# Performance work log

Measured on AMD Instinct MI355X. Metric: run time of the kernel, lower is better.

Reference implementation:

```python
import jax, jax.numpy as jnp
import numpy as np

D_MODEL = 1024
D_FFN = 4096
NUM_EXPERTS = 8
TOP_K = 2
EPS = 1e-7


def setup_inputs() -> dict:
    key = jax.random.key(0)
    ks = jax.random.split(key, 10)
    B, T = 2, 2048
    s = 0.02
    return {
        "x": jax.random.normal(ks[0], (B, T, D_MODEL), dtype=jnp.float32),
        "padding_mask": jnp.ones((B, T), dtype=bool),
        "rms_w": jnp.ones((D_MODEL,), dtype=jnp.float32),
        "router_w": jax.random.normal(ks[1], (NUM_EXPERTS, D_MODEL), dtype=jnp.float32) * s,
        "router_b": jnp.zeros((NUM_EXPERTS,), dtype=jnp.float32),
        "W1": jax.random.normal(ks[2], (NUM_EXPERTS, D_MODEL, D_FFN), dtype=jnp.float32) * s,
        "b1": jnp.zeros((NUM_EXPERTS, D_FFN), dtype=jnp.float32),
        "W2": jax.random.normal(ks[3], (NUM_EXPERTS, D_FFN, D_MODEL), dtype=jnp.float32) * s,
        "b2": jnp.zeros((NUM_EXPERTS, D_MODEL), dtype=jnp.float32),
        "W3": jax.random.normal(ks[4], (NUM_EXPERTS, D_MODEL, D_FFN), dtype=jnp.float32) * s,
        "b3": jnp.zeros((NUM_EXPERTS, D_FFN), dtype=jnp.float32),
    }


def reference(x, padding_mask, rms_w, router_w, router_b, W1, b1, W2, b2, W3, b3):
    B, T, d = x.shape
    # RMSNorm
    rms = jnp.sqrt(jnp.mean(x * x, axis=-1, keepdims=True) + EPS)
    xn = rms_w * (x / rms)
    xf = xn.reshape(-1, d)  # [N, d]

    # Router: softmax -> top-k -> renormalize
    logits = xf @ router_w.T + router_b            # [N, E]
    probs = jax.nn.softmax(logits, axis=-1)
    topv, topi = jax.lax.top_k(probs, TOP_K)       # [N, K]
    w = topv / jnp.sum(topv, axis=-1, keepdims=True)
    # Dense combine weights per (token, expert): sum of top-k weights routed to e
    combine = jnp.sum(jax.nn.one_hot(topi, NUM_EXPERTS, dtype=xf.dtype) * w[..., None], axis=1)  # [N, E]

    # Loop over experts via scan (one full-token SwiGLU FFN per expert, masked combine)
    def step(acc, params):
        W1e, b1e, W2e, b2e, W3e, b3e, ce = params
        h = jax.nn.silu(xf @ W1e + b1e) * (xf @ W3e + b3e)  # [N, d_ffn]
        y = h @ W2e + b2e                                    # [N, d]
        return acc + ce[:, None] * y, None

    out, _ = jax.lax.scan(step, jnp.zeros_like(xf), (W1, b1, W2, b2, W3, b3, combine.T))
    aux_loss = jnp.asarray(0.0, dtype=x.dtype)  # use_aux_loss only active in training mode
    return out.reshape(B, T, d), aux_loss
```

## Files before the change

kernel.cpp:

```cpp
#include <hip/hip_runtime.h>
#include <stdint.h>


#define NTOK 4096
#define DM   1024
#define DF   4096
#define NE   8
#define BM   128
#define MAX_RB 72
#define SLOT_CAP (MAX_RB * BM)

typedef _Float16 f16;
typedef __attribute__((ext_vector_type(8))) _Float16 f16x8;
typedef __attribute__((ext_vector_type(4))) _Float16 f16x4;
typedef __attribute__((ext_vector_type(4))) float    f32x4;
typedef __attribute__((ext_vector_type(2))) float    f32x2;

__device__ __forceinline__ void gl2lds16(const void* g, void* l) {
  __builtin_amdgcn_global_load_lds(
      (const __attribute__((address_space(1))) unsigned int*)g,
      (__attribute__((address_space(3))) unsigned int*)l, 16, 0, 0);
}

__global__ __launch_bounds__(256) void k_rms_router(
    const float* __restrict__ x, const float* __restrict__ rms_w,
    const float* __restrict__ rw, const float* __restrict__ rbias,
    f16* __restrict__ xn, int* __restrict__ topi, float* __restrict__ topw,
    int* __restrict__ counts)
{
  int t = blockIdx.x;
  int tid = threadIdx.x;
  const float* xr = x + (size_t)t * DM;
  f32x4 xv = *(const f32x4*)(xr + tid * 4);
  f32x4 gw = *(const f32x4*)(rms_w + tid * 4);
  f32x4 gv = xv * gw;

  float v[9];
  v[8] = xv[0]*xv[0] + xv[1]*xv[1] + xv[2]*xv[2] + xv[3]*xv[3];
#pragma unroll
  for (int e = 0; e < NE; ++e) {
    f32x4 wv = *(const f32x4*)(rw + e * DM + tid * 4);
    v[e] = gv[0]*wv[0] + gv[1]*wv[1] + gv[2]*wv[2] + gv[3]*wv[3];
  }
#pragma unroll
  for (int off = 32; off; off >>= 1) {
#pragma unroll
    for (int j = 0; j < 9; ++j) v[j] += __shfl_xor(v[j], off);
  }
  __shared__ float red[4][9];
  int wave = tid >> 6, lane = tid & 63;
  if (lane == 0) {
#pragma unroll
    for (int j = 0; j < 9; ++j) red[wave][j] = v[j];
  }
  __syncthreads();
  float tot[9];
#pragma unroll
  for (int j = 0; j < 9; ++j)
    tot[j] = red[0][j] + red[1][j] + red[2][j] + red[3][j];

  float rinv = 1.0f / sqrtf(tot[8] * (1.0f / DM) + 1e-7f);
  float lg[NE];
#pragma unroll
  for (int e = 0; e < NE; ++e) lg[e] = tot[e] * rinv + rbias[e];

  int e1 = 0; float b1v = lg[0];
#pragma unroll
  for (int e = 1; e < NE; ++e) if (lg[e] > b1v) { b1v = lg[e]; e1 = e; }
  int e2 = -1; float b2v = -1e30f;
#pragma unroll
  for (int e = 0; e < NE; ++e) if (e != e1 && lg[e] > b2v) { b2v = lg[e]; e2 = e; }

  float r2 = expf(b2v - b1v);
  float w1 = 1.0f / (1.0f + r2);
  float w2 = r2 * w1;

  if (tid == 0) {
    topi[t * 2 + 0] = e1; topi[t * 2 + 1] = e2;
    topw[t * 2 + 0] = w1; topw[t * 2 + 1] = w2;
    atomicAdd(&counts[e1], 1);
    atomicAdd(&counts[e2], 1);
  }
  f16x4 o;
#pragma unroll
  for (int i = 0; i < 4; ++i) o[i] = (f16)(gv[i] * rinv);
  *(f16x4*)(xn + (size_t)t * DM + tid * 4) = o;
}

__global__ void k_build(const int* __restrict__ counts, int* __restrict__ po,
                        int2* __restrict__ rbtable, int* __restrict__ total_rb)
{
  if (threadIdx.x != 0 || blockIdx.x != 0) return;
  int off = 0, idx = 0;
  for (int e = 0; e < NE; ++e) {
    int c = counts[e];
    po[e] = off;
    int nrb = (c + BM - 1) / BM;
    for (int r = 0; r < nrb; ++r) { rbtable[idx] = make_int2(e, off + r * BM); ++idx; }
    off += nrb * BM;
  }
  *total_rb = idx;
}

__global__ __launch_bounds__(256) void k_assign(
    const int* __restrict__ topi, const float* __restrict__ topw,
    const int* __restrict__ po, int* __restrict__ cursors,
    int* __restrict__ slot_token, float* __restrict__ slot_w,
    int* __restrict__ tok2slot)
{
  int t = blockIdx.x * 256 + threadIdx.x;
  if (t >= NTOK) return;
#pragma unroll
  for (int k = 0; k < 2; ++k) {
    int e = topi[t * 2 + k];
    int pos = atomicAdd(&cursors[e], 1);
    int slot = po[e] + pos;
    slot_token[slot] = t;
    slot_w[slot] = topw[t * 2 + k];
    tok2slot[t * 2 + k] = slot;
  }
}

__global__ __launch_bounds__(256) void k_convw(
    const float* __restrict__ W1, const float* __restrict__ W3,
    const float* __restrict__ W2, f16* __restrict__ w16)
{
  __shared__ f16 T[64][132];
  int g = blockIdx.x;
  int tensor = g >> 12;
  int rem = g & 4095;
  int e = rem >> 9;
  int t = rem & 511;
  const float* W; int nstride, np, kt;
  if (tensor == 2) { W = W2; nstride = DM; np = t >> 6; kt = t & 63; }
  else { W = (tensor == 0) ? W1 : W3; nstride = DF; np = t >> 4; kt = t & 15; }
  const float* src = W + (size_t)e * DM * DF + (size_t)(kt * 64) * nstride + np * 128;

  int tid = threadIdx.x;
  int q = tid & 31, kb = tid >> 5;
#pragma unroll
  for (int i = 0; i < 8; ++i) {
    int k = kb + 8 * i;
    f32x4 v = *(const f32x4*)(src + (size_t)k * nstride + q * 4);
    f16x4 h4 = { (f16)v[0], (f16)v[1], (f16)v[2], (f16)v[3] };
    *(f16x4*)(&T[k][q * 4]) = h4;
  }
  __syncthreads();
  int n = tid >> 1;
  f16* dst = w16 + ((size_t)(tensor * NE + e) * 512 + t) * 8192 + n * 64 + (tid & 1) * 32;
#pragma unroll
  for (int qq = 0; qq < 4; ++qq) {
    int cs = (tid & 1) * 4 + qq;
    int cl = cs ^ (n & 7);
    f16x8 o;
#pragma unroll
    for (int j = 0; j < 8; ++j) o[j] = T[cl * 8 + j][n];
    *(f16x8*)(dst + qq * 8) = o;
  }
}

__global__ __launch_bounds__(256, 3) void k_ffn13(
    const f16* __restrict__ xn, const int* __restrict__ slot_token,
    const int2* __restrict__ rbtable, const int* __restrict__ total_rb,
    const f16* __restrict__ w16,
    const float* __restrict__ b1, const float* __restrict__ b3,
    f16* __restrict__ h)
{
  int bid = blockIdx.x;
  int wl = (bid & 7) * 288 + (bid >> 3);
  int rbi = wl % 72;
  int np  = wl / 72;
  if (rbi >= *total_rb) return;
  int2 ent = rbtable[rbi];
  int e = ent.x, row0 = ent.y;
  int n0 = np * 128;

  __shared__ __align__(16) f16 As[128 * 64];
  __shared__ __align__(16) f16 Bs[2][128 * 64];

  int tid = threadIdx.x, lane = tid & 63, wave = tid >> 6;
  int wm = wave >> 1, wn = wave & 1;

  const f16* wb1 = w16 + ((size_t)(0 * NE + e) * 512 + np * 16) * 8192;
  const f16* wb3 = w16 + ((size_t)(1 * NE + e) * 512 + np * 16) * 8192;

  int tok[4];
#pragma unroll
  for (int q = 0; q < 4; ++q) {
    int m = q * 32 + wave * 8 + (lane >> 3);
    int tkn = slot_token[row0 + m];
    tok[q] = (tkn < 0) ? 0 : tkn;
  }
  int csx = (((lane & 7) ^ (lane >> 3)) << 3);
  int lin = wave * 512 + lane * 8;

  f32x4 acc1[4][4], acc3[4][4];
  f32x4 z = {0.f, 0.f, 0.f, 0.f};
#pragma unroll
  for (int i = 0; i < 4; ++i)
#pragma unroll
    for (int j = 0; j < 4; ++j) { acc1[i][j] = z; acc3[i][j] = z; }

  for (int kt = 0; kt < DM / 64; ++kt) {
    int k0 = kt * 64;
    const f16* s1 = wb1 + (size_t)kt * 8192;
    const f16* s3 = wb3 + (size_t)kt * 8192;
#pragma unroll
    for (int q = 0; q < 4; ++q) {
      gl2lds16(xn + (size_t)tok[q] * DM + k0 + csx,
               (char*)As + q * 4096 + wave * 1024);
      gl2lds16(s1 + q * 2048 + lin, (char*)Bs[0] + q * 4096 + wave * 1024);
      gl2lds16(s3 + q * 2048 + lin, (char*)Bs[1] + q * 4096 + wave * 1024);
    }
    __syncthreads();
#pragma unroll
    for (int kh = 0; kh < 2; ++kh) {
      int kk = kh * 32 + (lane >> 4) * 8;
      f16x8 a[4];
#pragma unroll
      for (int fm = 0; fm < 4; ++fm) {
        int m = wm * 64 + fm * 16 + (lane & 15);
        a[fm] = *(const f16x8*)((char*)As + m * 128 + 2 * (kk ^ ((m & 7) << 3)));
      }
#pragma unroll
      for (int fn = 0; fn < 4; ++fn) {
        int n = wn * 64 + fn * 16 + (lane & 15);
        f16x8 bf1 = *(const f16x8*)((char*)Bs[0] + n * 128 + 2 * (kk ^ ((n & 7) << 3)));
        f16x8 bf3 = *(const f16x8*)((char*)Bs[1] + n * 128 + 2 * (kk ^ ((n & 7) << 3)));
#pragma unroll
        for (int fm = 0; fm < 4; ++fm) {
          acc1[fm][fn] = __builtin_amdgcn_mfma_f32_16x16x32_f16(a[fm], bf1, acc1[fm][fn], 0, 0, 0);
          acc3[fm][fn] = __builtin_amdgcn_mfma_f32_16x16x32_f16(a[fm], bf3, acc3[fm][fn], 0, 0, 0);
        }
      }
    }
    __syncthreads();
  }
#pragma unroll
  for (int fn = 0; fn < 4; ++fn) {
    int nc = n0 + wn * 64 + fn * 16 + (lane & 15);
    float bb1 = b1[e * DF + nc], bb3 = b3[e * DF + nc];
#pragma unroll
    for (int fm = 0; fm < 4; ++fm) {
      int mbase = wm * 64 + fm * 16 + (lane >> 4) * 4;
#pragma unroll
      for (int r = 0; r < 4; ++r) {
        int sl = mbase + r;
        float u1 = acc1[fm][fn][r] + bb1;
        float u3 = acc3[fm][fn][r] + bb3;
        float hv = (u1 / (1.0f + __expf(-u1))) * u3;
        size_t off = (size_t)(row0 + sl) * DF + (nc & ~63)
                   + ((((nc >> 3) & 7) ^ (sl & 7)) << 3) + (nc & 7);
        h[off] = (f16)hv;
      }
    }
  }
}

__global__ __launch_bounds__(256, 4) void k_ffn2(
    const f16* __restrict__ h,
    const int2* __restrict__ rbtable, const int* __restrict__ total_rb,
    const f16* __restrict__ w16, f16* __restrict__ partial)
{
  int bid = blockIdx.x;
  int wl = (bid & 7) * 288 + (bid >> 3);
  int rbi = wl % 72;
  int rest = wl / 72;
  int kc = rest & 3;
  int np = rest >> 2;
  if (rbi >= *total_rb) return;
  int2 ent = rbtable[rbi];
  int e = ent.x, row0 = ent.y;
  int n0 = np * 128;

  __shared__ __align__(16) f16 As[128 * 64];
  __shared__ __align__(16) f16 Bsh[128 * 64];

  int tid = threadIdx.x, lane = tid & 63, wave = tid >> 6;
  int wm = wave >> 1, wn = wave & 1;
  const f16* wb = w16 + ((size_t)(2 * NE + e) * 512 + np * 64 + kc * 16) * 8192;
  int lin = wave * 512 + lane * 8;

  f32x4 acc[4][4];
  f32x4 z = {0.f, 0.f, 0.f, 0.f};
#pragma unroll
  for (int i = 0; i < 4; ++i)
#pragma unroll
    for (int j = 0; j < 4; ++j) acc[i][j] = z;

  for (int kt = 0; kt < 16; ++kt) {
    const f16* sB = wb + (size_t)kt * 8192;
    int k0 = kc * 1024 + kt * 64;
#pragma unroll
    for (int q = 0; q < 4; ++q) {
      int m = q * 32 + wave * 8 + (lane >> 3);
      gl2lds16(h + (size_t)(row0 + m) * DF + k0 + ((lane & 7) << 3),
               (char*)As + q * 4096 + wave * 1024);
      gl2lds16(sB + q * 2048 + lin, (char*)Bsh + q * 4096 + wave * 1024);
    }
    __syncthreads();
#pragma unroll
    for (int kh = 0; kh < 2; ++kh) {
      int kk = kh * 32 + (lane >> 4) * 8;
      f16x8 a[4];
#pragma unroll
      for (int fm = 0; fm < 4; ++fm) {
        int m = wm * 64 + fm * 16 + (lane & 15);
        a[fm] = *(const f16x8*)((char*)As + m * 128 + 2 * (kk ^ ((m & 7) << 3)));
      }
#pragma unroll
      for (int fn = 0; fn < 4; ++fn) {
        int n = wn * 64 + fn * 16 + (lane & 15);
        f16x8 bf = *(const f16x8*)((char*)Bsh + n * 128 + 2 * (kk ^ ((n & 7) << 3)));
#pragma unroll
        for (int fm = 0; fm < 4; ++fm)
          acc[fm][fn] = __builtin_amdgcn_mfma_f32_16x16x32_f16(a[fm], bf, acc[fm][fn], 0, 0, 0);
      }
    }
    __syncthreads();
  }
#pragma unroll
  for (int fn = 0; fn < 4; ++fn) {
    int nc = n0 + wn * 64 + fn * 16 + (lane & 15);
#pragma unroll
    for (int fm = 0; fm < 4; ++fm) {
      int mbase = wm * 64 + fm * 16 + (lane >> 4) * 4;
#pragma unroll
      for (int r = 0; r < 4; ++r) {
        int slot = row0 + mbase + r;
        partial[((size_t)(kc * SLOT_CAP + slot) << 10) + nc] = (f16)acc[fm][fn][r];
      }
    }
  }
}

__global__ __launch_bounds__(256) void k_combine(
    const f16* __restrict__ partial, const int* __restrict__ tok2slot,
    const int* __restrict__ topi, const float* __restrict__ topw,
    const float* __restrict__ b2, float* __restrict__ out)
{
  int t = blockIdx.x;
  int nc = threadIdx.x * 4;
  int s1 = tok2slot[t * 2], s2 = tok2slot[t * 2 + 1];
  float c1 = topw[t * 2], c2 = topw[t * 2 + 1];
  int e1 = topi[t * 2], e2 = topi[t * 2 + 1];
  float y1[4] = {0.f, 0.f, 0.f, 0.f}, y2[4] = {0.f, 0.f, 0.f, 0.f};
#pragma unroll
  for (int kc = 0; kc < 4; ++kc) {
    f16x4 p1 = *(const f16x4*)(partial + (((size_t)(kc * SLOT_CAP + s1)) << 10) + nc);
    f16x4 p2 = *(const f16x4*)(partial + (((size_t)(kc * SLOT_CAP + s2)) << 10) + nc);
#pragma unroll
    for (int i = 0; i < 4; ++i) { y1[i] += (float)p1[i]; y2[i] += (float)p2[i]; }
  }
  f32x4 bb1 = *(const f32x4*)(b2 + e1 * DM + nc);
  f32x4 bb2 = *(const f32x4*)(b2 + e2 * DM + nc);
  f32x4 o;
#pragma unroll
  for (int i = 0; i < 4; ++i)
    o[i] = c1 * (y1[i] + bb1[i]) + c2 * (y2[i] + bb2[i]);
  *(f32x4*)(out + ((size_t)t << 10) + nc) = o;
}

extern "C" void kernel_launch(void* const* d_in, const int* in_sizes, int n_in,
                              void* d_out, int out_size, void* d_ws, size_t ws_size,
                              hipStream_t stream)
{
  const float* x     = (const float*)d_in[0];
  const float* rms_w = (const float*)d_in[2];
  const float* rw    = (const float*)d_in[3];
  const float* rbias = (const float*)d_in[4];
  const float* W1    = (const float*)d_in[5];
  const float* b1    = (const float*)d_in[6];
  const float* W2    = (const float*)d_in[7];
  const float* b2    = (const float*)d_in[8];
  const float* W3    = (const float*)d_in[9];
  const float* b3    = (const float*)d_in[10];
  float* out = (float*)d_out;

  char* ws = (char*)d_ws;
  size_t o = 0;
  f16* w16 = (f16*)(ws + o); o += (size_t)3 * NE * 512 * 8192 * 2;
  f16* h   = (f16*)(ws + o); o += (size_t)SLOT_CAP * DF * 2;
  f16* xn  = (f16*)(ws + o); o += (size_t)NTOK * DM * 2;
  int*   slot_token = (int*)(ws + o);   o += SLOT_CAP * 4;
  float* slot_w     = (float*)(ws + o); o += SLOT_CAP * 4;
  int*   topi       = (int*)(ws + o);   o += NTOK * 2 * 4;
  float* topw       = (float*)(ws + o); o += NTOK * 2 * 4;
  int*   tok2slot   = (int*)(ws + o);   o += NTOK * 2 * 4;
  int*   counts     = (int*)(ws + o);   o += 64;
  int*   cursors    = (int*)(ws + o);   o += 64;
  int*   po         = (int*)(ws + o);   o += 64;
  int*   total_rb   = (int*)(ws + o);   o += 64;
  int2*  rbtable    = (int2*)(ws + o);  o += MAX_RB * 8;
  (void)ws_size; (void)in_sizes; (void)n_in;

  f16* partial = w16;

  hipMemsetAsync(d_out, 0, (size_t)out_size * 4, stream);
  hipMemsetAsync(counts, 0, 128, stream);
  hipMemsetAsync(slot_token, 0xFF, SLOT_CAP * 4, stream);

  k_convw<<<3 * NE * 512, 256, 0, stream>>>(W1, W3, W2, w16);
  k_rms_router<<<NTOK, 256, 0, stream>>>(x, rms_w, rw, rbias, xn, topi, topw, counts);
  k_build<<<1, 64, 0, stream>>>(counts, po, rbtable, total_rb);
  k_assign<<<16, 256, 0, stream>>>(topi, topw, po, cursors, slot_token, slot_w, tok2slot);
  k_ffn13<<<8 * 288, 256, 0, stream>>>(xn, slot_token, rbtable, total_rb,
                                       w16, b1, b3, h);
  k_ffn2<<<8 * 288, 256, 0, stream>>>(h, rbtable, total_rb, w16, partial);
  k_combine<<<NTOK, 256, 0, stream>>>(partial, tok2slot, topi, topw, b2, out);
}
```

Before: 548.7 us.

## Fuse W2 fp16 conversion into ffn13 and halve ffn2 split-K

Moves the W2 fp32-to-fp16 transpose/convert out of k_convw and into the tail of k_ffn13. Every ffn13 block, including ones with no routed work, converts two W2 tiles, which fills idle slots and overlaps conversion with the GEMM. k_ffn2 now uses 2 K-chunks instead of 4, halving its grid and the partial buffers read by combine. The trade-off is longer per-block K loops in ffn2 and less parallelism. Partial still aliases the W1/W3 region of w16, so W2 now sits in a separate slice.

```diff
diff --git a/kernel.cpp b/kernel.cpp
--- a/kernel.cpp
+++ b/kernel.cpp
@@ -123,7 +123,7 @@
 
 __global__ __launch_bounds__(256) void k_convw(
     const float* __restrict__ W1, const float* __restrict__ W3,
-    const float* __restrict__ W2, f16* __restrict__ w16)
+    f16* __restrict__ w16)
 {
   __shared__ f16 T[64][132];
   int g = blockIdx.x;
@@ -131,17 +131,16 @@
   int rem = g & 4095;
   int e = rem >> 9;
   int t = rem & 511;
-  const float* W; int nstride, np, kt;
-  if (tensor == 2) { W = W2; nstride = DM; np = t >> 6; kt = t & 63; }
-  else { W = (tensor == 0) ? W1 : W3; nstride = DF; np = t >> 4; kt = t & 15; }
-  const float* src = W + (size_t)e * DM * DF + (size_t)(kt * 64) * nstride + np * 128;
+  const float* W = (tensor == 0) ? W1 : W3;
+  int np = t >> 4, kt = t & 15;
+  const float* src = W + (size_t)e * DM * DF + (size_t)(kt * 64) * DF + np * 128;
 
   int tid = threadIdx.x;
   int q = tid & 31, kb = tid >> 5;
 #pragma unroll
   for (int i = 0; i < 8; ++i) {
     int k = kb + 8 * i;
-    f32x4 v = *(const f32x4*)(src + (size_t)k * nstride + q * 4);
+    f32x4 v = *(const f32x4*)(src + (size_t)k * DF + q * 4);
     f16x4 h4 = { (f16)v[0], (f16)v[1], (f16)v[2], (f16)v[3] };
     *(f16x4*)(&T[k][q * 4]) = h4;
   }
@@ -164,121 +163,154 @@
     const int2* __restrict__ rbtable, const int* __restrict__ total_rb,
     const f16* __restrict__ w16,
     const float* __restrict__ b1, const float* __restrict__ b3,
+    const float* __restrict__ W2, f16* __restrict__ w16_w2,
     f16* __restrict__ h)
 {
+  __shared__ __align__(16) f16 As[128 * 64];
+  __shared__ __align__(16) f16 Bs[2][128 * 64];
+
   int bid = blockIdx.x;
   int wl = (bid & 7) * 288 + (bid >> 3);
   int rbi = wl % 72;
   int np  = wl / 72;
+  int tid = threadIdx.x, lane = tid & 63, wave = tid >> 6;
+
+  bool active = (rbi < *total_rb);
+  if (active) {
+    int2 ent = rbtable[rbi];
+    int e = ent.x, row0 = ent.y;
+    int n0 = np * 128;
+
+    int wm = wave >> 1, wn = wave & 1;
+    const f16* wb1 = w16 + ((size_t)(0 * NE + e) * 512 + np * 16) * 8192;
+    const f16* wb3 = w16 + ((size_t)(1 * NE + e) * 512 + np * 16) * 8192;
+
+    int tok[4];
+#pragma unroll
+    for (int q = 0; q < 4; ++q) {
+      int m = q * 32 + wave * 8 + (lane >> 3);
+      int tkn = slot_token[row0 + m];
+      tok[q] = (tkn < 0) ? 0 : tkn;
+    }
+    int csx = (((lane & 7) ^ (lane >> 3)) << 3);
+    int lin = wave * 512 + lane * 8;
+
+    f32x4 acc1[4][4], acc3[4][4];
+    f32x4 z = {0.f, 0.f, 0.f, 0.f};
+#pragma unroll
+    for (int i = 0; i < 4; ++i)
+#pragma unroll
+      for (int j = 0; j < 4; ++j) { acc1[i][j] = z; acc3[i][j] = z; }
+
+    for (int kt = 0; kt < DM / 64; ++kt) {
+      int k0 = kt * 64;
+      const f16* s1 = wb1 + (size_t)kt * 8192;
+      const f16* s3 = wb3 + (size_t)kt * 8192;
+#pragma unroll
+      for (int q = 0; q < 4; ++q) {
+        gl2lds16(xn + (size_t)tok[q] * DM + k0 + csx,
+                 (char*)As + q * 4096 + wave * 1024);
+        gl2lds16(s1 + q * 2048 + lin, (char*)Bs[0] + q * 4096 + wave * 1024);
+        gl2lds16(s3 + q * 2048 + lin, (char*)Bs[1] + q * 4096 + wave * 1024);
+      }
+      __syncthreads();
+#pragma unroll
+      for (int kh = 0; kh < 2; ++kh) {
+        int kk = kh * 32 + (lane >> 4) * 8;
+        f16x8 a[4];
+#pragma unroll
+        for (int fm = 0; fm < 4; ++fm) {
+          int m = wm * 64 + fm * 16 + (lane & 15);
+          a[fm] = *(const f16x8*)((char*)As + m * 128 + 2 * (kk ^ ((m & 7) << 3)));
+        }
+#pragma unroll
+        for (int fn = 0; fn < 4; ++fn) {
+          int n = wn * 64 + fn * 16 + (lane & 15);
+          f16x8 bf1 = *(const f16x8*)((char*)Bs[0] + n * 128 + 2 * (kk ^ ((n & 7) << 3)));
+          f16x8 bf3 = *(const f16x8*)((char*)Bs[1] + n * 128 + 2 * (kk ^ ((n & 7) << 3)));
+#pragma unroll
+          for (int fm = 0; fm < 4; ++fm) {
+            acc1[fm][fn] = __builtin_amdgcn_mfma_f32_16x16x32_f16(a[fm], bf1, acc1[fm][fn], 0, 0, 0);
+            acc3[fm][fn] = __builtin_amdgcn_mfma_f32_16x16x32_f16(a[fm], bf3, acc3[fm][fn], 0, 0, 0);
+          }
+        }
+      }
+      __syncthreads();
+    }
+#pragma unroll
+    for (int fn = 0; fn < 4; ++fn) {
+      int nc = n0 + wn * 64 + fn * 16 + (lane & 15);
+      float bb1 = b1[e * DF + nc], bb3 = b3[e * DF + nc];
+#pragma unroll
+      for (int fm = 0; fm < 4; ++fm) {
+        int mbase = wm * 64 + fm * 16 + (lane >> 4) * 4;
+#pragma unroll
+        for (int r = 0; r < 4; ++r) {
+          int sl = mbase + r;
+          float u1 = acc1[fm][fn][r] + bb1;
+          float u3 = acc3[fm][fn][r] + bb3;
+          float hv = (u1 / (1.0f + __expf(-u1))) * u3;
+          size_t off = (size_t)(row0 + sl) * DF + (nc & ~63)
+                     + ((((nc >> 3) & 7) ^ (sl & 7)) << 3) + (nc & 7);
+          h[off] = (f16)hv;
+        }
+      }
+    }
+  }
+
+  f16 (*T)[132] = (f16(*)[132])(&Bs[0][0]);
+  int q = tid & 31, kb = tid >> 5;
+  for (int j = 0; j < 2; ++j) {
+    int tile = bid * 2 + j;
+    if (tile >= NE * 512) break;
+    int e2 = tile >> 9, t2 = tile & 511;
+    int np2 = t2 >> 6, kt2 = t2 & 63;
+    const float* src = W2 + (size_t)e2 * DM * DF + (size_t)(kt2 * 64) * DM + np2 * 128;
+    __syncthreads();
+#pragma unroll
+    for (int i = 0; i < 8; ++i) {
+      int k = kb + 8 * i;
+      f32x4 v = *(const f32x4*)(src + (size_t)k * DM + q * 4);
+      f16x4 h4 = { (f16)v[0], (f16)v[1], (f16)v[2], (f16)v[3] };
+      *(f16x4*)(&T[k][q * 4]) = h4;
+    }
+    __syncthreads();
+    int n = tid >> 1;
+    f16* dst = w16_w2 + (size_t)(e2 * 512 + t2) * 8192 + n * 64 + (tid & 1) * 32;
+#pragma unroll
+    for (int qq = 0; qq < 4; ++qq) {
+      int cs = (tid & 1) * 4 + qq;
+      int cl = cs ^ (n & 7);
+      f16x8 o8;
+#pragma unroll
+      for (int jj = 0; jj < 8; ++jj) o8[jj] = T[cl * 8 + jj][n];
+      *(f16x8*)(dst + qq * 8) = o8;
+    }
+  }
+}
+
+__global__ __launch_bounds__(256, 4) void k_ffn2(
+    const f16* __restrict__ h,
+    const int2* __restrict__ rbtable, const int* __restrict__ total_rb,
+    const f16* __restrict__ w16_w2, f16* __restrict__ partial)
+{
+  int bid = blockIdx.x;
+  int wl = (bid & 7) * 144 + (bid >> 3);
+  int rbi = wl % 72;
+  int rest = wl / 72;
+  int kc = rest & 1;
+  int np = rest >> 1;
   if (rbi >= *total_rb) return;
   int2 ent = rbtable[rbi];
   int e = ent.x, row0 = ent.y;
   int n0 = np * 128;
 
   __shared__ __align__(16) f16 As[128 * 64];
-  __shared__ __align__(16) f16 Bs[2][128 * 64];
+  __shared__ __align__(16) f16 Bsh[128 * 64];
 
   int tid = threadIdx.x, lane = tid & 63, wave = tid >> 6;
   int wm = wave >> 1, wn = wave & 1;
-
-  const f16* wb1 = w16 + ((size_t)(0 * NE + e) * 512 + np * 16) * 8192;
-  const f16* wb3 = w16 + ((size_t)(1 * NE + e) * 512 + np * 16) * 8192;
-
-  int tok[4];
-#pragma unroll
-  for (int q = 0; q < 4; ++q) {
-    int m = q * 32 + wave * 8 + (lane >> 3);
-    int tkn = slot_token[row0 + m];
-    tok[q] = (tkn < 0) ? 0 : tkn;
-  }
-  int csx = (((lane & 7) ^ (lane >> 3)) << 3);
-  int lin = wave * 512 + lane * 8;
-
-  f32x4 acc1[4][4], acc3[4][4];
-  f32x4 z = {0.f, 0.f, 0.f, 0.f};
-#pragma unroll
-  for (int i = 0; i < 4; ++i)
-#pragma unroll
-    for (int j = 0; j < 4; ++j) { acc1[i][j] = z; acc3[i][j] = z; }
-
-  for (int kt = 0; kt < DM / 64; ++kt) {
-    int k0 = kt * 64;
-    const f16* s1 = wb1 + (size_t)kt * 8192;
-    const f16* s3 = wb3 + (size_t)kt * 8192;
-#pragma unroll
-    for (int q = 0; q < 4; ++q) {
-      gl2lds16(xn + (size_t)tok[q] * DM + k0 + csx,
-               (char*)As + q * 4096 + wave * 1024);
-      gl2lds16(s1 + q * 2048 + lin, (char*)Bs[0] + q * 4096 + wave * 1024);
-      gl2lds16(s3 + q * 2048 + lin, (char*)Bs[1] + q * 4096 + wave * 1024);
-    }
-    __syncthreads();
-#pragma unroll
-    for (int kh = 0; kh < 2; ++kh) {
-      int kk = kh * 32 + (lane >> 4) * 8;
-      f16x8 a[4];
-#pragma unroll
-      for (int fm = 0; fm < 4; ++fm) {
-        int m = wm * 64 + fm * 16 + (lane & 15);
-        a[fm] = *(const f16x8*)((char*)As + m * 128 + 2 * (kk ^ ((m & 7) << 3)));
-      }
-#pragma unroll
-      for (int fn = 0; fn < 4; ++fn) {
-        int n = wn * 64 + fn * 16 + (lane & 15);
-        f16x8 bf1 = *(const f16x8*)((char*)Bs[0] + n * 128 + 2 * (kk ^ ((n & 7) << 3)));
-        f16x8 bf3 = *(const f16x8*)((char*)Bs[1] + n * 128 + 2 * (kk ^ ((n & 7) << 3)));
-#pragma unroll
-        for (int fm = 0; fm < 4; ++fm) {
-          acc1[fm][fn] = __builtin_amdgcn_mfma_f32_16x16x32_f16(a[fm], bf1, acc1[fm][fn], 0, 0, 0);
-          acc3[fm][fn] = __builtin_amdgcn_mfma_f32_16x16x32_f16(a[fm], bf3, acc3[fm][fn], 0, 0, 0);
-        }
-      }
-    }
-    __syncthreads();
-  }
-#pragma unroll
-  for (int fn = 0; fn < 4; ++fn) {
-    int nc = n0 + wn * 64 + fn * 16 + (lane & 15);
-    float bb1 = b1[e * DF + nc], bb3 = b3[e * DF + nc];
-#pragma unroll
-    for (int fm = 0; fm < 4; ++fm) {
-      int mbase = wm * 64 + fm * 16 + (lane >> 4) * 4;
-#pragma unroll
-      for (int r = 0; r < 4; ++r) {
-        int sl = mbase + r;
-        float u1 = acc1[fm][fn][r] + bb1;
-        float u3 = acc3[fm][fn][r] + bb3;
-        float hv = (u1 / (1.0f + __expf(-u1))) * u3;
-        size_t off = (size_t)(row0 + sl) * DF + (nc & ~63)
-                   + ((((nc >> 3) & 7) ^ (sl & 7)) << 3) + (nc & 7);
-        h[off] = (f16)hv;
-      }
-    }
-  }
-}
-
-__global__ __launch_bounds__(256, 4) void k_ffn2(
-    const f16* __restrict__ h,
-    const int2* __restrict__ rbtable, const int* __restrict__ total_rb,
-    const f16* __restrict__ w16, f16* __restrict__ partial)
-{
-  int bid = blockIdx.x;
-  int wl = (bid & 7) * 288 + (bid >> 3);
-  int rbi = wl % 72;
-  int rest = wl / 72;
-  int kc = rest & 3;
-  int np = rest >> 2;
-  if (rbi >= *total_rb) return;
-  int2 ent = rbtable[rbi];
-  int e = ent.x, row0 = ent.y;
-  int n0 = np * 128;
-
-  __shared__ __align__(16) f16 As[128 * 64];
-  __shared__ __align__(16) f16 Bsh[128 * 64];
-
-  int tid = threadIdx.x, lane = tid & 63, wave = tid >> 6;
-  int wm = wave >> 1, wn = wave & 1;
-  const f16* wb = w16 + ((size_t)(2 * NE + e) * 512 + np * 64 + kc * 16) * 8192;
+  const f16* wb = w16_w2 + ((size_t)e * 512 + np * 64 + kc * 32) * 8192;
   int lin = wave * 512 + lane * 8;
 
   f32x4 acc[4][4];
@@ -288,9 +320,9 @@
 #pragma unroll
     for (int j = 0; j < 4; ++j) acc[i][j] = z;
 
-  for (int kt = 0; kt < 16; ++kt) {
+  for (int kt = 0; kt < 32; ++kt) {
     const f16* sB = wb + (size_t)kt * 8192;
-    int k0 = kc * 1024 + kt * 64;
+    int k0 = kc * 2048 + kt * 64;
 #pragma unroll
     for (int q = 0; q < 4; ++q) {
       int m = q * 32 + wave * 8 + (lane >> 3);
@@ -346,7 +378,7 @@
   int e1 = topi[t * 2], e2 = topi[t * 2 + 1];
   float y1[4] = {0.f, 0.f, 0.f, 0.f}, y2[4] = {0.f, 0.f, 0.f, 0.f};
 #pragma unroll
-  for (int kc = 0; kc < 4; ++kc) {
+  for (int kc = 0; kc < 2; ++kc) {
     f16x4 p1 = *(const f16x4*)(partial + (((size_t)(kc * SLOT_CAP + s1)) << 10) + nc);
     f16x4 p2 = *(const f16x4*)(partial + (((size_t)(kc * SLOT_CAP + s2)) << 10) + nc);
 #pragma unroll
@@ -394,18 +426,20 @@
   int2*  rbtable    = (int2*)(ws + o);  o += MAX_RB * 8;
   (void)ws_size; (void)in_sizes; (void)n_in;
 
+  f16* w16_w2 = w16 + (size_t)2 * NE * 512 * 8192;
+
   f16* partial = w16;
 
   hipMemsetAsync(d_out, 0, (size_t)out_size * 4, stream);
   hipMemsetAsync(counts, 0, 128, stream);
   hipMemsetAsync(slot_token, 0xFF, SLOT_CAP * 4, stream);
 
-  k_convw<<<3 * NE * 512, 256, 0, stream>>>(W1, W3, W2, w16);
+  k_convw<<<2 * NE * 512, 256, 0, stream>>>(W1, W3, w16);
   k_rms_router<<<NTOK, 256, 0, stream>>>(x, rms_w, rw, rbias, xn, topi, topw, counts);
   k_build<<<1, 64, 0, stream>>>(counts, po, rbtable, total_rb);
   k_assign<<<16, 256, 0, stream>>>(topi, topw, po, cursors, slot_token, slot_w, tok2slot);
   k_ffn13<<<8 * 288, 256, 0, stream>>>(xn, slot_token, rbtable, total_rb,
-                                       w16, b1, b3, h);
-  k_ffn2<<<8 * 288, 256, 0, stream>>>(h, rbtable, total_rb, w16, partial);
+                                       w16, b1, b3, W2, w16_w2, h);
+  k_ffn2<<<8 * 144, 256, 0, stream>>>(h, rbtable, total_rb, w16_w2, partial);
   k_combine<<<NTOK, 256, 0, stream>>>(partial, tok2slot, topi, topw, b2, out);
 }
```

New measurement: 536.3 us. -2.2%, faster.
